# Kernel tuning notes

Hardware: AMD Instinct MI355X
Metric: run time of the kernel (lower is better)

The kernel has to match this reference:

```python
import jax, jax.numpy as jnp
import numpy as np

B, T, E = 64, 1024, 2048  # BATCH_SIZE, TRAIN_LEN, EMBEDDING_LEN (E > T branch, as in repo configs)


def setup_inputs() -> dict:
    key = jax.random.key(0)
    delay_embedding = jax.random.normal(key, (B, T, E), dtype=jnp.float32)
    return {"delay_embedding": delay_embedding}


def reference(delay_embedding):
    """Hankel anti-diagonal segmented mean (embedding_2_predict_y, all_y=False).

    delay_embedding: [B, T, E]. Elements with equal index-sum s = i + j lie on the
    same anti-diagonal; the torch code averages each such diagonal. With
    all_y=False it returns diagonals s = T .. T+E-2  ->  output shape [B, E-1].
    One fused segment_sum pass replaces the per-batch, per-diagonal python loops.
    """
    Bv, Tv, Ev = delay_embedding.shape
    S = Tv + Ev - 1  # number of anti-diagonals
    seg = (jnp.arange(Tv)[:, None] + jnp.arange(Ev)[None, :]).reshape(-1)  # [T*E]
    data = delay_embedding.reshape(Bv, Tv * Ev).T  # [T*E, B], segments on axis 0
    sums = jax.ops.segment_sum(data, seg, num_segments=S)  # [S, B]
    counts = jax.ops.segment_sum(jnp.ones((Tv * Ev,), jnp.float32), seg, num_segments=S)  # [S]
    means = (sums / counts[:, None]).T  # [B, S]
    return means[:, Tv:]  # [B, E-1]
```

## Files before the change

kernel.cpp:

```cpp
#include <hip/hip_runtime.h>


#define T_LEN 1024
#define E_LEN 2048
#define K_OUT (E_LEN - 1)
#define B_SZ  64
#define NBLK  (28 * B_SZ)

__global__ void __launch_bounds__(256)
diag_accum(const float* __restrict__ in, float* __restrict__ out) {
    __shared__ float lacc[1024];

    const int b  = blockIdx.x & (B_SZ - 1);
    const int u2 = blockIdx.x >> 6;

    int G, rcb;
    if (u2 < 8)       { G = 0; rcb = u2 * 2;            }
    else if (u2 < 16) { G = 1; rcb = (u2 - 8) * 2;      }
    else if (u2 < 24) { G = 2; rcb = (u2 - 16) * 2;     }
    else              { G = 3; rcb = 8 + (u2 - 24) * 2; }

    const int w    = threadIdx.x >> 6;
    const int lane = threadIdx.x & 63;
    const int rc   = rcb + (w >> 1);
    const int p    = w & 1;

    const int k0 = G * 512 + p * 256 + (lane << 2);
    const int r0 = rc * 64;
    const int r1 = r0 + 64;

    int il0       = max(r0, k0     - (T_LEN - 1));
    const int il3 = max(r0, k0 + 3 - (T_LEN - 1));

    float sx = 0.f, sy = 0.f, sz = 0.f, sw = 0.f;
    if (il0 < r1) {
        const float* pp = in + (size_t)b * T_LEN * E_LEN
                             + (size_t)il0 * (E_LEN - 1)
                             + (size_t)(T_LEN + k0);
        int i = il0;

        const int head_end = min(il3, r1);
        for (; i < head_end; ++i) {
            sx += pp[0];
            if (i >= k0 + 1 - (T_LEN - 1)) sy += pp[1];
            if (i >= k0 + 2 - (T_LEN - 1)) sz += pp[2];
            pp += (E_LEN - 1);
        }

        #pragma unroll 8
        for (; i < r1; ++i) {
            float v[4];
            __builtin_memcpy(v, pp, 16);
            sx += v[0]; sy += v[1]; sz += v[2]; sw += v[3];
            pp += (E_LEN - 1);
        }
    }

    float4* dst = (float4*)&lacc[w * 256 + (lane << 2)];
    *dst = make_float4(sx, sy, sz, sw);
    __syncthreads();

    #pragma unroll 2
    for (int t = threadIdx.x; t < 512; t += 256) {
        const int k = G * 512 + t;
        if (k < K_OUT) {
            const float v = lacc[t] + lacc[512 + t];
            const int cnt = T_LEN - max(0, k - (T_LEN - 1));
            unsafeAtomicAdd(&out[(size_t)b * K_OUT + k], v * (1.0f / (float)cnt));
        }
    }
}

extern "C" void kernel_launch(void* const* d_in, const int* in_sizes, int n_in,
                              void* d_out, int out_size, void* d_ws, size_t ws_size,
                              hipStream_t stream) {
    const float* in = (const float*)d_in[0];
    float* out = (float*)d_out;

    hipMemsetAsync(out, 0, sizeof(float) * B_SZ * K_OUT, stream);

    diag_accum<<<NBLK, 256, 0, stream>>>(in, out);
}
```

Baseline: 86.03 us.

## Give each wave a full 512-column strip with 8 columns per lane and pair triangular row chunks

```diff
diff --git a/kernel.cpp b/kernel.cpp
--- a/kernel.cpp
+++ b/kernel.cpp
@@ -7,66 +7,86 @@
 #define B_SZ  64
 #define NBLK  (28 * B_SZ)
 
-__global__ void __launch_bounds__(256)
+__global__ void __launch_bounds__(256, 7)
 diag_accum(const float* __restrict__ in, float* __restrict__ out) {
-    __shared__ float lacc[1024];
+    __shared__ float lacc[2048];
 
-    const int b  = blockIdx.x & (B_SZ - 1);
-    const int u2 = blockIdx.x >> 6;
-
-    int G, rcb;
-    if (u2 < 8)       { G = 0; rcb = u2 * 2;            }
-    else if (u2 < 16) { G = 1; rcb = (u2 - 8) * 2;      }
-    else if (u2 < 24) { G = 2; rcb = (u2 - 16) * 2;     }
-    else              { G = 3; rcb = 8 + (u2 - 24) * 2; }
-
+    const int b    = blockIdx.x & (B_SZ - 1);
+    const int u2   = blockIdx.x >> 6;
     const int w    = threadIdx.x >> 6;
     const int lane = threadIdx.x & 63;
-    const int rc   = rcb + (w >> 1);
-    const int p    = w & 1;
 
-    const int k0 = G * 512 + p * 256 + (lane << 2);
-    const int r0 = rc * 64;
-    const int r1 = r0 + 64;
+    int G, rc;
+    bool light = false;
+    if (u2 < 8)       { G = 0; rc = (u2 << 2) | w; }
+    else if (u2 < 16) { G = 1; rc = ((u2 - 8) << 2) | w; }
+    else if (u2 < 20) { G = 2; rc = 16 + ((u2 - 16) << 2) + w; }
+    else {
+        light = true;
+        const int l = u2 - 20;
+        if (w == 0)      { G = 2; rc = 2 * l;      }
+        else if (w == 1) { G = 2; rc = 2 * l + 1;  }
+        else if (w == 2) { G = 3; rc = 31 - 2 * l; }
+        else             { G = 3; rc = 30 - 2 * l; }
+    }
 
-    int il0       = max(r0, k0     - (T_LEN - 1));
-    const int il3 = max(r0, k0 + 3 - (T_LEN - 1));
+    const int k0 = (G << 9) + (lane << 3);
+    const int r0 = rc << 5;
+    const int r1 = r0 + 32;
 
-    float sx = 0.f, sy = 0.f, sz = 0.f, sw = 0.f;
+    const int il0 = max(r0, k0 - (T_LEN - 1));
+    int ilc       = max(r0, k0 - (T_LEN - 1) + 7);
+    if (ilc > r1) ilc = r1;
+
+    float s[8] = {0.f, 0.f, 0.f, 0.f, 0.f, 0.f, 0.f, 0.f};
     if (il0 < r1) {
-        const float* pp = in + (size_t)b * T_LEN * E_LEN
-                             + (size_t)il0 * (E_LEN - 1)
-                             + (size_t)(T_LEN + k0);
+        const float* p = in + (size_t)b * T_LEN * E_LEN
+                            + (size_t)il0 * (E_LEN - 1)
+                            + (size_t)(T_LEN + k0);
         int i = il0;
 
-        const int head_end = min(il3, r1);
-        for (; i < head_end; ++i) {
-            sx += pp[0];
-            if (i >= k0 + 1 - (T_LEN - 1)) sy += pp[1];
-            if (i >= k0 + 2 - (T_LEN - 1)) sz += pp[2];
-            pp += (E_LEN - 1);
+        for (; i < ilc; ++i) {
+            const int mc = i + (T_LEN - 1) - k0;
+            #pragma unroll
+            for (int c = 0; c < 8; ++c)
+                if (c <= mc) s[c] += p[c];
+            p += (E_LEN - 1);
         }
 
-        #pragma unroll 8
+        #pragma unroll 2
         for (; i < r1; ++i) {
-            float v[4];
-            __builtin_memcpy(v, pp, 16);
-            sx += v[0]; sy += v[1]; sz += v[2]; sw += v[3];
-            pp += (E_LEN - 1);
+            float v0[4], v1[4];
+            __builtin_memcpy(v0, p,     16);
+            __builtin_memcpy(v1, p + 4, 16);
+            s[0] += v0[0]; s[1] += v0[1]; s[2] += v0[2]; s[3] += v0[3];
+            s[4] += v1[0]; s[5] += v1[1]; s[6] += v1[2]; s[7] += v1[3];
+            p += (E_LEN - 1);
         }
     }
 
-    float4* dst = (float4*)&lacc[w * 256 + (lane << 2)];
-    *dst = make_float4(sx, sy, sz, sw);
+    float4* dst = (float4*)&lacc[(w << 9) + (lane << 3)];
+    dst[0] = make_float4(s[0], s[1], s[2], s[3]);
+    dst[1] = make_float4(s[4], s[5], s[6], s[7]);
     __syncthreads();
 
-    #pragma unroll 2
-    for (int t = threadIdx.x; t < 512; t += 256) {
-        const int k = G * 512 + t;
-        if (k < K_OUT) {
-            const float v = lacc[t] + lacc[512 + t];
+    if (!light) {
+        #pragma unroll 2
+        for (int t = threadIdx.x; t < 512; t += 256) {
+            const int k = (G << 9) + t;
+            const float v = lacc[t] + lacc[512 + t] + lacc[1024 + t] + lacc[1536 + t];
             const int cnt = T_LEN - max(0, k - (T_LEN - 1));
             unsafeAtomicAdd(&out[(size_t)b * K_OUT + k], v * (1.0f / (float)cnt));
+        }
+    } else {
+        #pragma unroll 4
+        for (int t = threadIdx.x; t < 1024; t += 256) {
+            const int seg = t >> 9, tl = t & 511;
+            const int k = 1024 + (seg << 9) + tl;
+            if (k < K_OUT) {
+                const float v = lacc[(seg << 10) + tl] + lacc[(seg << 10) + 512 + tl];
+                const int cnt = T_LEN - max(0, k - (T_LEN - 1));
+                unsafeAtomicAdd(&out[(size_t)b * K_OUT + k], v * (1.0f / (float)cnt));
+            }
         }
     }
 }
```

Result: slower. 88.74 us (+3.2%).
